# Performance work log

Hardware: AMD Instinct MI355X
Metric: run time of the kernel (lower is better)

The kernel has to match this reference:

```python
import jax, jax.numpy as jnp
import numpy as np
import math

D_MODEL = 1024
NUM_HEADS = 16
HEAD_DIM = D_MODEL // NUM_HEADS
BATCH = 2
SEQ = 2048
THETA = 10000.0


def _rope_tables(seq_len, head_dim, theta=THETA):
    inv_freq = 1.0 / theta ** (jnp.arange(0, head_dim, 2, dtype=jnp.float32) / head_dim)
    pos = jnp.arange(seq_len, dtype=jnp.float32)
    freqs = jnp.outer(pos, inv_freq)                 # [S, hd/2]
    emb = jnp.concatenate([freqs, freqs], axis=-1)   # [S, hd]
    return jnp.cos(emb), jnp.sin(emb)


def _rotate_half(x):
    x1, x2 = jnp.split(x, 2, axis=-1)
    return jnp.concatenate([-x2, x1], axis=-1)


def setup_inputs() -> dict:
    key = jax.random.key(0)
    k1, k2, k3 = jax.random.split(key, 3)
    x = jax.random.normal(k1, (BATCH, SEQ, D_MODEL), dtype=jnp.float32)
    # causal mask: 1 where attend allowed, 0 where masked
    mask = jnp.tril(jnp.ones((SEQ, SEQ), dtype=jnp.int32))[None, None]
    w_qkv = jax.random.normal(k2, (D_MODEL, 3 * D_MODEL), dtype=jnp.float32) / math.sqrt(D_MODEL)
    w_out = jax.random.normal(k3, (D_MODEL, D_MODEL), dtype=jnp.float32) / math.sqrt(D_MODEL)
    return {"x": x, "mask": mask, "w_qkv": w_qkv, "w_out": w_out}


def reference(x, mask, w_qkv, w_out):
    B, S, _ = x.shape
    qkv = x @ w_qkv                                          # [B,S,3*D]
    qkv = qkv.reshape(B, S, 3, NUM_HEADS, HEAD_DIM)
    qkv = jnp.transpose(qkv, (2, 0, 3, 1, 4))                # [3,B,H,S,hd]
    q, k, v = qkv[0], qkv[1], qkv[2]
    cos, sin = _rope_tables(S, HEAD_DIM)                     # [S,hd]
    cos = cos[None, None]; sin = sin[None, None]
    q = q * cos + _rotate_half(q) * sin
    k = k * cos + _rotate_half(k) * sin
    scores = jnp.einsum('bhqd,bhkd->bhqk', q, k) / math.sqrt(HEAD_DIM)
    scores = jnp.where(mask == 0, -jnp.inf, scores)
    attn = jax.nn.softmax(scores, axis=-1)                   # dropout p=0 (eval)
    out = jnp.einsum('bhqk,bhkd->bhqd', attn, v)             # [B,H,S,hd]
    out = jnp.transpose(out, (0, 2, 1, 3)).reshape(B, S, D_MODEL)
    return out @ w_out
```

## Files before the change

### kernel.cpp

```cpp
#include <hip/hip_runtime.h>

typedef __bf16 bf16;
typedef __bf16 bf16x4 __attribute__((ext_vector_type(4)));
typedef __bf16 bf16x8 __attribute__((ext_vector_type(8)));
typedef short s16x4 __attribute__((ext_vector_type(4)));
typedef float f32x4 __attribute__((ext_vector_type(4)));

constexpr int BATCH = 2;
constexpr int SEQ   = 2048;
constexpr int DMODEL= 1024;
constexpr int NH    = 16;
constexpr int HD    = 64;
constexpr int M_ROWS= BATCH * SEQ;
constexpr int N_QKV = 3 * DMODEL;

#if defined(__HIP_DEVICE_COMPILE__) && __has_builtin(__builtin_amdgcn_exp2f)
#define EXP2(x) __builtin_amdgcn_exp2f(x)
#else
#define EXP2(x) exp2f(x)
#endif

__device__ __forceinline__ void gl_lds16(const bf16* g, bf16* l) {
  __builtin_amdgcn_global_load_lds(
      (const __attribute__((address_space(1))) unsigned int*)g,
      (__attribute__((address_space(3))) unsigned int*)l, 16, 0, 0);
}

__device__ __forceinline__ f32x4 mfma_16x16x16_bf16(bf16x4 a, bf16x4 b,
                                                    f32x4 c) {
#if defined(__HIP_DEVICE_COMPILE__)
  union { bf16x4 h; s16x4 s; } ua{a}, ub{b};
  return __builtin_amdgcn_mfma_f32_16x16x16bf16_1k(ua.s, ub.s, c, 0, 0, 0);
#else
  return c;
#endif
}

__global__ __launch_bounds__(256) void prep_kernel(
    const float* __restrict__ x, const float* __restrict__ w_qkv,
    const float* __restrict__ w_out, bf16* __restrict__ xb,
    bf16* __restrict__ WqkvT, bf16* __restrict__ WoutT) {
  const int bx = blockIdx.x, t = threadIdx.x;
  if (bx < 2048) {
    const int i = (bx * 256 + t) * 8;
    float4 f0 = *(const float4*)&x[i];
    float4 f1 = *(const float4*)&x[i + 4];
    bf16x8 v;
    v[0] = (bf16)f0.x; v[1] = (bf16)f0.y; v[2] = (bf16)f0.z; v[3] = (bf16)f0.w;
    v[4] = (bf16)f1.x; v[5] = (bf16)f1.y; v[6] = (bf16)f1.z; v[7] = (bf16)f1.w;
    *(bf16x8*)&xb[i] = v;
    return;
  }
  __shared__ float tile[32][33];
  const float* src;
  bf16* dst;
  int R, C, c0, r0;
  if (bx < 5120) {
    const int idx = bx - 2048;
    src = w_qkv; dst = WqkvT; R = DMODEL; C = N_QKV;
    c0 = (idx % 96) * 32; r0 = (idx / 96) * 32;
  } else {
    const int idx = bx - 5120;
    src = w_out; dst = WoutT; R = DMODEL; C = DMODEL;
    c0 = (idx & 31) * 32; r0 = (idx >> 5) * 32;
  }
  const int r = t >> 3, c4 = (t & 7) * 4;
  {
    float4 f = *(const float4*)&src[(size_t)(r0 + r) * C + c0 + c4];
    tile[r][c4 + 0] = f.x; tile[r][c4 + 1] = f.y;
    tile[r][c4 + 2] = f.z; tile[r][c4 + 3] = f.w;
  }
  __syncthreads();
  {
    bf16x4 v;
#pragma unroll
    for (int j = 0; j < 4; j++) v[j] = (bf16)tile[c4 + j][r];
    *(bf16x4*)&dst[(size_t)(c0 + r) * R + r0 + c4] = v;
  }
}

#define GEMM_BODY(A, BT, K)                                                    \
  __shared__ bf16 smem[8448];                                                  \
  bf16* As = smem;                                                             \
  bf16* Bs = smem + 4096;                                                      \
  const int t = threadIdx.x;                                                   \
  const int m0 = blockIdx.y * 128;                                             \
  const int n0 = blockIdx.x * 128;                                             \
  const int w = t >> 6, lane = t & 63, g = lane >> 4, li = lane & 15;          \
  const int r0w = (w & 1) * 64, c0w = (w >> 1) * 64;                           \
  f32x4 acc[4][4] = {};                                                        \
  for (int k0 = 0; k0 < (K); k0 += 32) {                                       \
    __syncthreads();                                                           \
    _Pragma("unroll") for (int c = 0; c < 2; c++) {                            \
      const int idx = (w * 2 + c) * 64 + lane;                                 \
      const int row = idx >> 2, col = (idx & 3) * 8;                           \
      gl_lds16(&(A)[(size_t)(m0 + row) * (K) + k0 + col],                      \
               &As[(w * 2 + c) * 512]);                                        \
      gl_lds16(&(BT)[(size_t)(n0 + row) * (K) + k0 + col],                     \
               &Bs[(w * 2 + c) * 512]);                                        \
    }                                                                          \
    __syncthreads();                                                           \
    bf16x8 a[4], b[4];                                                         \
    _Pragma("unroll") for (int mt = 0; mt < 4; mt++)                           \
        a[mt] = *(const bf16x8*)&As[(r0w + mt * 16 + li) * 32 + g * 8];        \
    _Pragma("unroll") for (int nt = 0; nt < 4; nt++)                           \
        b[nt] = *(const bf16x8*)&Bs[(c0w + nt * 16 + li) * 32 + g * 8];        \
    _Pragma("unroll") for (int mt = 0; mt < 4; mt++)                           \
        _Pragma("unroll") for (int nt = 0; nt < 4; nt++)                       \
            acc[mt][nt] = __builtin_amdgcn_mfma_f32_16x16x32_bf16(             \
                a[mt], b[nt], acc[mt][nt], 0, 0, 0);                           \
  }

__global__ __launch_bounds__(256) void gemm_out64(
    const bf16* __restrict__ A, const bf16* __restrict__ BT,
    float* __restrict__ C, int M, int N, int K) {
  __shared__ bf16 As[64 * 32];
  __shared__ bf16 Bs[128 * 32];
  const int t = threadIdx.x;
  const int m0 = blockIdx.y * 64;
  const int n0 = blockIdx.x * 128;
  const int w = t >> 6, lane = t & 63, g = lane >> 4, li = lane & 15;
  const int r0w = (w & 1) * 32, c0w = (w >> 1) * 64;
  f32x4 acc[2][4] = {};
  for (int k0 = 0; k0 < K; k0 += 32) {
    __syncthreads();
    {
      const int idx = w * 64 + lane;
      const int row = idx >> 2, col = (idx & 3) * 8;
      gl_lds16(&A[(size_t)(m0 + row) * K + k0 + col], &As[w * 512]);
    }
#pragma unroll
    for (int c = 0; c < 2; c++) {
      const int idx = (w * 2 + c) * 64 + lane;
      const int row = idx >> 2, col = (idx & 3) * 8;
      gl_lds16(&BT[(size_t)(n0 + row) * K + k0 + col], &Bs[(w * 2 + c) * 512]);
    }
    __syncthreads();
    bf16x8 a[2], b[4];
#pragma unroll
    for (int mt = 0; mt < 2; mt++)
      a[mt] = *(const bf16x8*)&As[(r0w + mt * 16 + li) * 32 + g * 8];
#pragma unroll
    for (int nt = 0; nt < 4; nt++)
      b[nt] = *(const bf16x8*)&Bs[(c0w + nt * 16 + li) * 32 + g * 8];
#pragma unroll
    for (int mt = 0; mt < 2; mt++)
#pragma unroll
      for (int nt = 0; nt < 4; nt++)
        acc[mt][nt] = __builtin_amdgcn_mfma_f32_16x16x32_bf16(
            a[mt], b[nt], acc[mt][nt], 0, 0, 0);
  }
#pragma unroll
  for (int mt = 0; mt < 2; mt++)
#pragma unroll
    for (int nt = 0; nt < 4; nt++)
#pragma unroll
      for (int r = 0; r < 4; r++) {
        const int m = m0 + r0w + mt * 16 + g * 4 + r;
        const int n = n0 + c0w + nt * 16 + li;
        C[(size_t)m * N + n] = acc[mt][nt][r];
      }
}

__global__ __launch_bounds__(256) void gemm_qkv_rope(
    const bf16* __restrict__ A, const bf16* __restrict__ BT,
    bf16* __restrict__ Qb, bf16* __restrict__ Kb, bf16* __restrict__ Vt) {
  constexpr int K = DMODEL;
  GEMM_BODY(A, BT, K)

  const int region = n0 >> 10;
  const int b = m0 >> 11;
  const int h = ((n0 + c0w) >> 6) & 15;
  const size_t bh = (size_t)(b * NH + h);

  if (region < 2) {
    bf16* dst = region == 0 ? Qb : Kb;
    const float outsc = region == 0 ? 0.125f * 1.44269504f : 1.f;
    const float L = 13.287712379549449f;
    const float if0 = exp2f(-(float)(2 * li) / 64.f * L);
    const float if1 = exp2f(-(float)(2 * (li + 16)) / 64.f * L);
    bf16* lw = smem + w * 2112;
#pragma unroll
    for (int pass = 0; pass < 2; pass++) {
      __syncthreads();
#pragma unroll
      for (int mtl = 0; mtl < 2; mtl++) {
        const int mt = pass * 2 + mtl;
#pragma unroll
        for (int r = 0; r < 4; r++) {
          const int s = (m0 + r0w + mt * 16 + g * 4 + r) & (SEQ - 1);
          float cs[2], sn[2];
          __sincosf((float)s * if0, &sn[0], &cs[0]);
          __sincosf((float)s * if1, &sn[1], &cs[1]);
#pragma unroll
          for (int nt = 0; nt < 4; nt++) {
            const int par = nt & 1;
            const float a = acc[mt][nt][r];
            const float ap = acc[mt][nt ^ 2][r];
            const float v = (nt < 2) ? a * cs[par] - ap * sn[par]
                                     : a * cs[par] + ap * sn[par];
            lw[(mtl * 16 + g * 4 + r) * 66 + nt * 16 + li] =
                (bf16)(v * outsc);
          }
        }
      }
      __syncthreads();
      const int rowl = lane >> 1, dh = (lane & 1) * 32;
      const int s = (m0 + r0w + pass * 32 + rowl) & (SEQ - 1);
      bf16* gdst = &dst[(bh * SEQ + s) * HD + dh];
      const bf16* lsrc = &lw[rowl * 66 + dh];
#pragma unroll
      for (int c = 0; c < 4; c++)
        *(bf16x8*)&gdst[c * 8] = *(const bf16x8*)&lsrc[c * 8];
    }
  } else {
#pragma unroll
    for (int mt = 0; mt < 4; mt++)
#pragma unroll
      for (int nt = 0; nt < 4; nt++) {
        const int s = (m0 + r0w + mt * 16 + g * 4) & (SEQ - 1);
        const int d = nt * 16 + li;
        bf16x4 v;
#pragma unroll
        for (int r = 0; r < 4; r++) v[r] = (bf16)acc[mt][nt][r];
        *(bf16x4*)&Vt[(bh * HD + d) * SEQ + s] = v;
      }
  }
}

__device__ const unsigned char CHUNK_TAB[80] = {
    124, 125, 126, 127,
    120, 121, 122, 116, 117, 118, 112, 113, 114, 108, 109, 110,
    104, 105, 106, 100, 101, 102, 96,  97,  98,  92,  93,  94,
    88,  89,  84,  85,  80,  81,  76,  77,  72,  73,  68,  69,
    64,  65,  60,  61,
    56,  52,  48,  44,  40,  36,  32,  28,
    24,  57,  90,  123, 20,  53,  86,  119, 16,  49,  82,  115,
    12,  45,  78,  111, 8,   41,  74,  107, 4,   37,  70,  103,
    0,   33,  66,  99};

__global__ __launch_bounds__(256, 5) void flash_attn15(
    const bf16* __restrict__ Q, const bf16* __restrict__ Kb,
    const bf16* __restrict__ Vt, bf16* __restrict__ Oout,
    float* __restrict__ Opart, float* __restrict__ Lpart) {
  const int bx = blockIdx.x;
  const unsigned char e = CHUNK_TAB[bx >> 5];
  const int qt = e >> 2, kch = e & 3;
  const int bh = bx & 31;
  const int q0 = qt * 64;
  const int jlo = kch * 8;
  const int jhi = min(jlo + 8, qt + 1);
  const int t = threadIdx.x, w = t >> 6, lane = t & 63, g = lane >> 4,
            li = lane & 15;

  __shared__ bf16 Ks[2][4096];
  __shared__ bf16 Vs[2][4096];

  const bf16* Qh = Q  + (size_t)bh * SEQ * HD;
  const bf16* Kh = Kb + (size_t)bh * SEQ * HD;
  const bf16* Vh = Vt + (size_t)bh * HD * SEQ;

  const int qw = q0 + w * 16;

  bf16x8 qf[2];
#pragma unroll
  for (int ks = 0; ks < 2; ks++)
    qf[ks] = *(const bf16x8*)&Qh[(size_t)(qw + li) * HD + ks * 32 + g * 8];

  f32x4 o[4] = {};
  f32x4 o4  = {};
  bf16x4 ones;
#pragma unroll
  for (int r = 0; r < 4; r++) ones[r] = (bf16)1.f;

  int koffB[2][4];
#pragma unroll
  for (int ks = 0; ks < 2; ks++)
#pragma unroll
    for (int nt = 0; nt < 4; nt++) {
      const int rK = nt * 16 + li;
      const int pK = rK * 8 + ((ks * 4 + g) ^ (li & 7));
      koffB[ks][nt] = pK * 16;
    }
  int voffB[4][4];
#pragma unroll
  for (int nt = 0; nt < 4; nt++)
#pragma unroll
    for (int dt = 0; dt < 4; dt++) {
      const int rV = dt * 16 + li;
      const int cg = nt * 2 + (g >> 1);
      const int pV = rV * 8 + (cg ^ (rV & 7));
      voffB[nt][dt] = pV * 16 + (g & 1) * 8;
    }

  const int p0 = w * 128 + lane, p1 = p0 + 64;
  const int sr0 = p0 >> 3, sc0 = ((p0 & 7) ^ (sr0 & 7)) * 8;
  const int sr1 = p1 >> 3, sc1 = ((p1 & 7) ^ (sr1 & 7)) * 8;
  const int lo0 = w * 1024, lo1 = w * 1024 + 512;

  {
    const int jn = jlo * 64;
    gl_lds16(&Kh[(size_t)(jn + sr0) * HD + sc0], &Ks[jlo & 1][lo0]);
    gl_lds16(&Kh[(size_t)(jn + sr1) * HD + sc1], &Ks[jlo & 1][lo1]);
    gl_lds16(&Vh[(size_t)sr0 * SEQ + jn + sc0], &Vs[jlo & 1][lo0]);
    gl_lds16(&Vh[(size_t)sr1 * SEQ + jn + sc1], &Vs[jlo & 1][lo1]);
  }
  __syncthreads();

  for (int ti = jlo; ti < jhi; ++ti) {
    const int cur = ti & 1, nxt = cur ^ 1;
    const char* ksb = (const char*)&Ks[cur][0];
    const char* vsb = (const char*)&Vs[cur][0];
    if (ti + 1 < jhi) {
      const int jn = ti * 64 + 64;
      gl_lds16(&Kh[(size_t)(jn + sr0) * HD + sc0], &Ks[nxt][lo0]);
      gl_lds16(&Kh[(size_t)(jn + sr1) * HD + sc1], &Ks[nxt][lo1]);
      gl_lds16(&Vh[(size_t)sr0 * SEQ + jn + sc0], &Vs[nxt][lo0]);
      gl_lds16(&Vh[(size_t)sr1 * SEQ + jn + sc1], &Vs[nxt][lo1]);
    }

    if (ti < qt) {
      f32x4 sacc[4] = {};
      __builtin_amdgcn_s_setprio(1);
#pragma unroll
      for (int ks = 0; ks < 2; ks++)
#pragma unroll
        for (int nt = 0; nt < 4; nt++) {
          bf16x8 kf = *(const bf16x8*)(ksb + koffB[ks][nt]);
          sacc[nt] = __builtin_amdgcn_mfma_f32_16x16x32_bf16(kf, qf[ks],
                                                             sacc[nt], 0, 0, 0);
        }
      __builtin_amdgcn_s_setprio(0);

      bf16x4 pf[4];
#pragma unroll
      for (int nt = 0; nt < 4; nt++)
#pragma unroll
        for (int r = 0; r < 4; r++) pf[nt][r] = (bf16)EXP2(sacc[nt][r]);

      __builtin_amdgcn_s_setprio(1);
#pragma unroll
      for (int nt = 0; nt < 4; nt++) {
        o4 = mfma_16x16x16_bf16(ones, pf[nt], o4);
#pragma unroll
        for (int dt = 0; dt < 4; dt++) {
          bf16x4 vfrag = *(const bf16x4*)(vsb + voffB[nt][dt]);
          o[dt] = mfma_16x16x16_bf16(vfrag, pf[nt], o[dt]);
        }
      }
      __builtin_amdgcn_s_setprio(0);
    } else {
      f32x4 sacc[4] = {};
      __builtin_amdgcn_s_setprio(1);
#pragma unroll
      for (int ks = 0; ks < 2; ks++)
#pragma unroll
        for (int nt = 0; nt < 4; nt++) {
          if (nt > w) continue;
          bf16x8 kf = *(const bf16x8*)(ksb + koffB[ks][nt]);
          sacc[nt] = __builtin_amdgcn_mfma_f32_16x16x32_bf16(kf, qf[ks],
                                                             sacc[nt], 0, 0, 0);
        }
      __builtin_amdgcn_s_setprio(0);

      bf16x4 pf[4];
#pragma unroll
      for (int nt = 0; nt < 4; nt++) {
        if (nt > w) continue;
#pragma unroll
        for (int r = 0; r < 4; r++) {
          float v = sacc[nt][r];
          if (nt == w) {
            const int kk = nt * 16 + g * 4 + r;
            v = (kk <= w * 16 + li) ? v : -1e30f;
          }
          pf[nt][r] = (bf16)EXP2(v);
        }
      }

      __builtin_amdgcn_s_setprio(1);
#pragma unroll
      for (int nt = 0; nt < 4; nt++) {
        if (nt > w) continue;
        o4 = mfma_16x16x16_bf16(ones, pf[nt], o4);
#pragma unroll
        for (int dt = 0; dt < 4; dt++) {
          bf16x4 vfrag = *(const bf16x4*)(vsb + voffB[nt][dt]);
          o[dt] = mfma_16x16x16_bf16(vfrag, pf[nt], o[dt]);
        }
      }
      __builtin_amdgcn_s_setprio(0);
    }
    __syncthreads();
  }

  if (qt <= 7) {
    const float inv_l = 1.f / o4[0];
    const int b = bh >> 4, h = bh & 15;
    const int s = qw + li;
#pragma unroll
    for (int dt = 0; dt < 4; dt++) {
      bf16x4 ov;
#pragma unroll
      for (int r = 0; r < 4; r++) ov[r] = (bf16)(o[dt][r] * inv_l);
      *(bf16x4*)&Oout[((size_t)(b * SEQ + s)) * DMODEL + h * 64 + dt * 16 +
                      g * 4] = ov;
    }
  } else {
    const int s = qw + li;
    int off;
    if (qt < 16)       off = (s - 512) * 2 + kch;
    else if (qt < 24)  off = 1024 + (s - 1024) * 3 + kch;
    else               off = 2560 + (s - 1536) * 4 + kch;
    const size_t slot = (size_t)bh * 4608 + off;
    if (g == 0) Lpart[slot] = o4[0];
    float* od = &Opart[slot * 64];
#pragma unroll
    for (int dt = 0; dt < 4; dt++)
      *(f32x4*)&od[dt * 16 + g * 4] = o[dt];
  }
}

__global__ __launch_bounds__(256) void attn_merge2(
    const float* __restrict__ Opart, const float* __restrict__ Lpart,
    bf16* __restrict__ attn) {
  const int gi = blockIdx.x * 256 + threadIdx.x;
  const int row = gi >> 3;
  const int d0 = (gi & 7) * 8;
  const int bh = row / 1536, srel = row - bh * 1536;
  const int b = bh >> 4, h = bh & 15, s = srel + 512;
  int off0, nc;
  if (srel < 512)       { off0 = srel * 2;                nc = 2; }
  else if (srel < 1024) { off0 = 1024 + (srel - 512) * 3; nc = 3; }
  else                  { off0 = 2560 + (srel - 1024) * 4; nc = 4; }
  const size_t base = (size_t)bh * 4608 + off0;
  float lsum = 0.f;
  float acc[8] = {};
  for (int c = 0; c < nc; c++) {
    lsum += Lpart[base + c];
    const float* p = &Opart[(base + c) * 64 + d0];
    float4 a0 = *(const float4*)p;
    float4 a1 = *(const float4*)(p + 4);
    acc[0] += a0.x; acc[1] += a0.y; acc[2] += a0.z; acc[3] += a0.w;
    acc[4] += a1.x; acc[5] += a1.y; acc[6] += a1.z; acc[7] += a1.w;
  }
  const float inv = 1.f / lsum;
  bf16x8 v;
#pragma unroll
  for (int i = 0; i < 8; i++) v[i] = (bf16)(acc[i] * inv);
  *(bf16x8*)&attn[((size_t)(b * SEQ + s)) * DMODEL + h * 64 + d0] = v;
}

extern "C" void kernel_launch(void* const* d_in, const int* in_sizes, int n_in,
                              void* d_out, int out_size, void* d_ws,
                              size_t ws_size, hipStream_t stream) {
  const float* x     = (const float*)d_in[0];
  const float* w_qkv = (const float*)d_in[2];
  const float* w_out = (const float*)d_in[3];
  float* out = (float*)d_out;

  char* ws = (char*)d_ws;
  bf16* WqkvT = (bf16*)(ws);
  bf16* WoutT = (bf16*)(ws + 6291456);
  bf16* xb    = (bf16*)(ws + 8388608);
  bf16* Qb    = (bf16*)(ws + 16777216);
  bf16* Kbuf  = (bf16*)(ws + 25165824);
  bf16* Vt    = (bf16*)(ws + 33554432);
  bf16* attn  = (bf16*)(ws + 41943040);
  float* Opart= (float*)(ws + 50331648);
  float* Lpart= (float*)(ws + 88080384);

  prep_kernel<<<dim3(6144), 256, 0, stream>>>(x, w_qkv, w_out, xb, WqkvT,
                                              WoutT);
  gemm_qkv_rope<<<dim3(N_QKV / 128, M_ROWS / 128), 256, 0, stream>>>(
      xb, WqkvT, Qb, Kbuf, Vt);
  flash_attn15<<<dim3(2560), 256, 0, stream>>>(Qb, Kbuf, Vt, attn, Opart,
                                               Lpart);
  attn_merge2<<<dim3(1536), 256, 0, stream>>>(Opart, Lpart, attn);
  gemm_out64<<<dim3(DMODEL / 128, M_ROWS / 64), 256, 0, stream>>>(
      attn, WoutT, out, M_ROWS, DMODEL, DMODEL);
}
```

Baseline: 192.3 us.

## Double-buffer LDS tiles in QKV and output GEMMs to overlap loads with MFMA

```diff
diff --git a/kernel.cpp b/kernel.cpp
--- a/kernel.cpp
+++ b/kernel.cpp
@@ -79,77 +79,54 @@
   }
 }
 
-#define GEMM_BODY(A, BT, K)                                                    \
-  __shared__ bf16 smem[8448];                                                  \
-  bf16* As = smem;                                                             \
-  bf16* Bs = smem + 4096;                                                      \
-  const int t = threadIdx.x;                                                   \
-  const int m0 = blockIdx.y * 128;                                             \
-  const int n0 = blockIdx.x * 128;                                             \
-  const int w = t >> 6, lane = t & 63, g = lane >> 4, li = lane & 15;          \
-  const int r0w = (w & 1) * 64, c0w = (w >> 1) * 64;                           \
-  f32x4 acc[4][4] = {};                                                        \
-  for (int k0 = 0; k0 < (K); k0 += 32) {                                       \
-    __syncthreads();                                                           \
-    _Pragma("unroll") for (int c = 0; c < 2; c++) {                            \
-      const int idx = (w * 2 + c) * 64 + lane;                                 \
-      const int row = idx >> 2, col = (idx & 3) * 8;                           \
-      gl_lds16(&(A)[(size_t)(m0 + row) * (K) + k0 + col],                      \
-               &As[(w * 2 + c) * 512]);                                        \
-      gl_lds16(&(BT)[(size_t)(n0 + row) * (K) + k0 + col],                     \
-               &Bs[(w * 2 + c) * 512]);                                        \
-    }                                                                          \
-    __syncthreads();                                                           \
-    bf16x8 a[4], b[4];                                                         \
-    _Pragma("unroll") for (int mt = 0; mt < 4; mt++)                           \
-        a[mt] = *(const bf16x8*)&As[(r0w + mt * 16 + li) * 32 + g * 8];        \
-    _Pragma("unroll") for (int nt = 0; nt < 4; nt++)                           \
-        b[nt] = *(const bf16x8*)&Bs[(c0w + nt * 16 + li) * 32 + g * 8];        \
-    _Pragma("unroll") for (int mt = 0; mt < 4; mt++)                           \
-        _Pragma("unroll") for (int nt = 0; nt < 4; nt++)                       \
-            acc[mt][nt] = __builtin_amdgcn_mfma_f32_16x16x32_bf16(             \
-                a[mt], b[nt], acc[mt][nt], 0, 0, 0);                           \
-  }
-
 __global__ __launch_bounds__(256) void gemm_out64(
     const bf16* __restrict__ A, const bf16* __restrict__ BT,
     float* __restrict__ C, int M, int N, int K) {
-  __shared__ bf16 As[64 * 32];
-  __shared__ bf16 Bs[128 * 32];
+  __shared__ bf16 As[2][2048];
+  __shared__ bf16 Bs[2][4096];
   const int t = threadIdx.x;
   const int m0 = blockIdx.y * 64;
   const int n0 = blockIdx.x * 128;
   const int w = t >> 6, lane = t & 63, g = lane >> 4, li = lane & 15;
   const int r0w = (w & 1) * 32, c0w = (w >> 1) * 64;
   f32x4 acc[2][4] = {};
-  for (int k0 = 0; k0 < K; k0 += 32) {
-    __syncthreads();
-    {
-      const int idx = w * 64 + lane;
-      const int row = idx >> 2, col = (idx & 3) * 8;
-      gl_lds16(&A[(size_t)(m0 + row) * K + k0 + col], &As[w * 512]);
-    }
-#pragma unroll
-    for (int c = 0; c < 2; c++) {
-      const int idx = (w * 2 + c) * 64 + lane;
-      const int row = idx >> 2, col = (idx & 3) * 8;
-      gl_lds16(&BT[(size_t)(n0 + row) * K + k0 + col], &Bs[(w * 2 + c) * 512]);
-    }
-    __syncthreads();
+  const int ia = w * 64 + lane;
+  const int ra = ia >> 2, ca = (ia & 3) * 8;
+  const int ib0 = (w * 2 + 0) * 64 + lane, ib1 = (w * 2 + 1) * 64 + lane;
+  const int rb0 = ib0 >> 2, cb0 = (ib0 & 3) * 8;
+  const int rb1 = ib1 >> 2, cb1 = (ib1 & 3) * 8;
+
+#define OUT_STAGE(buf, k0)                                                   \
+  {                                                                          \
+    gl_lds16(&A[(size_t)(m0 + ra) * K + (k0) + ca], &As[buf][w * 512]);      \
+    gl_lds16(&BT[(size_t)(n0 + rb0) * K + (k0) + cb0],                       \
+             &Bs[buf][(w * 2 + 0) * 512]);                                   \
+    gl_lds16(&BT[(size_t)(n0 + rb1) * K + (k0) + cb1],                       \
+             &Bs[buf][(w * 2 + 1) * 512]);                                   \
+  }
+
+  OUT_STAGE(0, 0);
+  __syncthreads();
+  for (int it = 0; it < 32; ++it) {
+    const int cur = it & 1;
+    if (it < 31) OUT_STAGE(cur ^ 1, (it + 1) * 32);
     bf16x8 a[2], b[4];
 #pragma unroll
     for (int mt = 0; mt < 2; mt++)
-      a[mt] = *(const bf16x8*)&As[(r0w + mt * 16 + li) * 32 + g * 8];
+      a[mt] = *(const bf16x8*)&As[cur][(r0w + mt * 16 + li) * 32 + g * 8];
 #pragma unroll
     for (int nt = 0; nt < 4; nt++)
-      b[nt] = *(const bf16x8*)&Bs[(c0w + nt * 16 + li) * 32 + g * 8];
+      b[nt] = *(const bf16x8*)&Bs[cur][(c0w + nt * 16 + li) * 32 + g * 8];
 #pragma unroll
     for (int mt = 0; mt < 2; mt++)
 #pragma unroll
       for (int nt = 0; nt < 4; nt++)
         acc[mt][nt] = __builtin_amdgcn_mfma_f32_16x16x32_bf16(
             a[mt], b[nt], acc[mt][nt], 0, 0, 0);
-  }
+    __syncthreads();
+  }
+#undef OUT_STAGE
+
 #pragma unroll
   for (int mt = 0; mt < 2; mt++)
 #pragma unroll
@@ -166,7 +143,55 @@
     const bf16* __restrict__ A, const bf16* __restrict__ BT,
     bf16* __restrict__ Qb, bf16* __restrict__ Kb, bf16* __restrict__ Vt) {
   constexpr int K = DMODEL;
-  GEMM_BODY(A, BT, K)
+  __shared__ bf16 smem[16384];
+  const int t = threadIdx.x;
+  const int m0 = blockIdx.y * 128;
+  const int n0 = blockIdx.x * 128;
+  const int w = t >> 6, lane = t & 63, g = lane >> 4, li = lane & 15;
+  const int r0w = (w & 1) * 64, c0w = (w >> 1) * 64;
+  f32x4 acc[4][4] = {};
+
+  const int i0 = (w * 2 + 0) * 64 + lane, i1 = (w * 2 + 1) * 64 + lane;
+  const int sr0 = i0 >> 2, sc0 = (i0 & 3) * 8;
+  const int sr1 = i1 >> 2, sc1 = (i1 & 3) * 8;
+
+#define QKV_STAGE(buf, k0)                                                   \
+  {                                                                          \
+    bf16* Asb = smem + (buf)*4096;                                           \
+    bf16* Bsb = smem + 8192 + (buf)*4096;                                    \
+    gl_lds16(&A[(size_t)(m0 + sr0) * K + (k0) + sc0],                        \
+             &Asb[(w * 2 + 0) * 512]);                                       \
+    gl_lds16(&A[(size_t)(m0 + sr1) * K + (k0) + sc1],                        \
+             &Asb[(w * 2 + 1) * 512]);                                       \
+    gl_lds16(&BT[(size_t)(n0 + sr0) * K + (k0) + sc0],                       \
+             &Bsb[(w * 2 + 0) * 512]);                                       \
+    gl_lds16(&BT[(size_t)(n0 + sr1) * K + (k0) + sc1],                       \
+             &Bsb[(w * 2 + 1) * 512]);                                       \
+  }
+
+  QKV_STAGE(0, 0);
+  __syncthreads();
+  for (int it = 0; it < 32; ++it) {
+    const int cur = it & 1;
+    if (it < 31) QKV_STAGE(cur ^ 1, (it + 1) * 32);
+    const bf16* Asb = smem + cur * 4096;
+    const bf16* Bsb = smem + 8192 + cur * 4096;
+    bf16x8 a[4], b[4];
+#pragma unroll
+    for (int mt = 0; mt < 4; mt++)
+      a[mt] = *(const bf16x8*)&Asb[(r0w + mt * 16 + li) * 32 + g * 8];
+#pragma unroll
+    for (int nt = 0; nt < 4; nt++)
+      b[nt] = *(const bf16x8*)&Bsb[(c0w + nt * 16 + li) * 32 + g * 8];
+#pragma unroll
+    for (int mt = 0; mt < 4; mt++)
+#pragma unroll
+      for (int nt = 0; nt < 4; nt++)
+        acc[mt][nt] = __builtin_amdgcn_mfma_f32_16x16x32_bf16(
+            a[mt], b[nt], acc[mt][nt], 0, 0, 0);
+    __syncthreads();
+  }
+#undef QKV_STAGE
 
   const int region = n0 >> 10;
   const int b = m0 >> 11;
```

Measured after the change: 194.2 us. No clear change (+1.0%).
